# Optimization experiments

Hardware: AMD Instinct MI355X
Metric: run time of the kernel (lower is better)

Reference implementation:

```python
import jax, jax.numpy as jnp
import numpy as np


def setup_inputs() -> dict:
    key = jax.random.key(0)
    k1, k2, k3, k4, k5 = jax.random.split(key, 5)
    B, IN_N, POSE = 32, 8192, 64
    M = 8                     # matrix_pose_dim = sqrt(64)
    NH, S2, HID = 32, 256, 256  # in_n/(img^2), img^2, hidden_dim
    OUT_N = 64
    return {
        "current_pose": jax.random.normal(k1, (B, IN_N, POSE), jnp.float32),
        "w_current": 0.02 * jax.random.normal(k2, (1, 1, IN_N, M, M), jnp.float32),
        "w_next": 0.02 * jax.random.normal(k3, (OUT_N, M, M), jnp.float32),
        "E_proj": 0.02 * jax.random.normal(k4, (NH, S2, HID), jnp.float32),
        "rel_embedd": jax.random.normal(k5, (1, 1, POSE), jnp.float32),
    }


def reference(current_pose, w_current, w_next, E_proj, rel_embedd):
    B, IN_N, POSE = current_pose.shape
    M = w_current.shape[-1]           # matrix_pose_dim
    NH, S2, HID = E_proj.shape        # heads, img*img, hidden_dim
    OUT_N = w_next.shape[0]

    # w_current: (1,1,IN_N,M,M) -> (1,IN_N,M,M); per-capsule pose-matrix multiply
    wc = w_current.reshape(IN_N, M, M)[None]
    cp = current_pose.reshape(B, IN_N, M, M)
    cp = jnp.matmul(cp, wc)                      # (B, IN_N, M, M)

    # raw reshape (row-major, matches torch .reshape) then Linformer projection
    cp = cp.reshape(B, POSE, NH, 1, S2)
    cp = jnp.matmul(cp, E_proj)                  # (B, POSE, NH, 1, HID)
    cp = cp[:, :, :, 0, :]                       # squeeze(3) -> (B, POSE, NH, HID)
    cp = cp.reshape(B, NH * HID, POSE)           # raw reshape as in torch

    # dots = softmax over out_n axis of a constant tensor == uniform 1/OUT_N.
    # einsum('bij,bje->bie') with uniform dots == mean over j, broadcast over i.
    pooled = jnp.sum(cp, axis=1, keepdims=True) / OUT_N   # (B, 1, POSE)
    npc = jnp.broadcast_to(pooled, (B, OUT_N, POSE))

    # add relative embedding (h_out = w_out = output_img_size = 1)
    npc = npc.reshape(B, OUT_N, 1, 1, POSE) + rel_embedd  # (B,OUT_N,1,1,POSE)
    npc = jnp.transpose(npc, (0, 2, 3, 1, 4)).reshape(B, OUT_N, POSE)

    # next-layer pose-matrix multiply
    npc = npc.reshape(B, OUT_N, M, M)
    npc = jnp.matmul(npc, w_next[None])           # (B, OUT_N, M, M)
    npc = npc.reshape(B, 1, 1, OUT_N, POSE)
    return npc[:, 0]                              # squeeze(1) -> (B,1,OUT_N,POSE)
```

## Files before the change

kernel.cpp:

```cpp
#include <hip/hip_runtime.h>
#include <hip/hip_bf16.h>


typedef short short8_t __attribute__((ext_vector_type(8)));
typedef float f32x4_t __attribute__((ext_vector_type(4)));
typedef int   int4_t  __attribute__((ext_vector_type(4)));

__device__ __forceinline__ short f2bf(float f) {
    union { float f; unsigned u; } v; v.f = f;
    unsigned r = v.u + 0x7FFFu + ((v.u >> 16) & 1u);
    return (short)(r >> 16);
}

__device__ __forceinline__ int cvt_pk(float x, float y) {
    int r;
    asm("v_cvt_pk_bf16_f32 %0, %1, %2" : "=v"(r) : "v"(x), "v"(y));
    return r;
}

__global__ void k_prep(const float* __restrict__ WC, short* __restrict__ WCf,
                       const float* __restrict__ E, float* __restrict__ F) {
    if (blockIdx.x < 256) {
        int t   = blockIdx.x * 256 + threadIdx.x;
        int l   = t & 63;
        int pc  = (t >> 6) & 15;
        int rp  = t >> 10;
        int lhi = l >> 4;
        int j   = l & 15;
        int row = (pc * 4 + lhi) * 128 + rp * 2 + (j >> 3);
        const float* src = WC + ((size_t)row << 6) + (j & 7);
        short8_t o;
        #pragma unroll
        for (int k = 0; k < 8; ++k) o[k] = f2bf(src[k * 8]);
        ((short8_t*)WCf)[t] = o;
    } else {
        int idx = ((blockIdx.x - 256) * 256 + threadIdx.x) * 4;
        int q   = idx & 63;
        int row = idx >> 6;
        int r   = row >> 6;
        int e   = row & 63;
        int nh  = r >> 2;
        int s2  = ((r & 3) << 6) + e;
        const float* base = E + (((size_t)nh * 256 + s2) << 8) + q;
        float4 s0 = *(const float4*)(base);
        float4 s1 = *(const float4*)(base + 64);
        float4 s2v = *(const float4*)(base + 128);
        float4 s3 = *(const float4*)(base + 192);
        float4 o;
        o.x = s0.x + s1.x + s2v.x + s3.x;
        o.y = s0.y + s1.y + s2v.y + s3.y;
        o.z = s0.z + s1.z + s2v.z + s3.z;
        o.w = s0.w + s1.w + s2v.w + s3.w;
        *(float4*)(F + idx) = o;
    }
}

__global__ void __launch_bounds__(512, 4)
k_bc(const float* __restrict__ CP, const short* __restrict__ WCf,
     const float* __restrict__ F, float* __restrict__ P) {
    int gx   = blockIdx.x;
    int half = gx & 1;
    int rpg  = gx >> 1;
    int b0   = blockIdx.y * 2;
    int w = threadIdx.x >> 6;
    int l = threadIdx.x & 63;
    int b_loc  = w & 1;
    int rp_loc = w >> 1;
    int rp = rpg * 4 + rp_loc;
    int r0 = rp * 2;
    int b  = b0 + b_loc;

    int i16   = l & 15;
    int r_sel = i16 >> 3;
    int m1    = i16 & 7;
    int lhi   = l >> 4;

    __shared__ float Stile[2][512];
    __shared__ float redp[8][2][64];

    const float* cp_base = CP + ((size_t)b << 19) + ((size_t)(r0 + r_sel) << 6) + m1 * 8;
    const short8_t* wf   = (const short8_t*)WCf + (size_t)rp * 1024 + (half * 8) * 64 + l;

    short8_t wr0 = wf[0 * 64], wr1 = wf[1 * 64], wr2 = wf[2 * 64], wr3 = wf[3 * 64];
    short8_t wr4 = wf[4 * 64], wr5 = wf[5 * 64], wr6 = wf[6 * 64], wr7 = wf[7 * 64];

    const float* pbase = cp_base + (((size_t)(half * 8) * 4 + lhi) << 13);
    #define CPA(c) (pbase + ((size_t)((c) * 4) << 13))

    float4 a0A, a1A, b0A, b1A;
    float4 a0B, a1B, b0B, b1B;
    float4 a0C, a1C, b0C, b1C;
    float4 a0D, a1D, b0D, b1D;

    a0A = *(const float4*)(CPA(0));     a1A = *(const float4*)(CPA(0) + 4);
    b0A = *(const float4*)(CPA(1));     b1A = *(const float4*)(CPA(1) + 4);
    a0B = *(const float4*)(CPA(2));     a1B = *(const float4*)(CPA(2) + 4);
    b0B = *(const float4*)(CPA(3));     b1B = *(const float4*)(CPA(3) + 4);

    f32x4_t acc0 = {0.f, 0.f, 0.f, 0.f};
    f32x4_t acc1 = {0.f, 0.f, 0.f, 0.f};

    #define DO_PAIR(x0, x1, y0, y1, wlo, whi)                                  \
    {                                                                          \
        int4_t ai, bi;                                                         \
        ai[0] = cvt_pk(x0.x, x0.y); ai[1] = cvt_pk(x0.z, x0.w);                \
        ai[2] = cvt_pk(x1.x, x1.y); ai[3] = cvt_pk(x1.z, x1.w);                \
        bi[0] = cvt_pk(y0.x, y0.y); bi[1] = cvt_pk(y0.z, y0.w);                \
        bi[2] = cvt_pk(y1.x, y1.y); bi[3] = cvt_pk(y1.z, y1.w);                \
        acc0 = __builtin_amdgcn_mfma_f32_16x16x32_bf16(                        \
            __builtin_bit_cast(short8_t, ai), wlo, acc0, 0, 0, 0);             \
        acc1 = __builtin_amdgcn_mfma_f32_16x16x32_bf16(                        \
            __builtin_bit_cast(short8_t, bi), whi, acc1, 0, 0, 0);             \
    }

    a0C = *(const float4*)(CPA(4));     a1C = *(const float4*)(CPA(4) + 4);
    b0C = *(const float4*)(CPA(5));     b1C = *(const float4*)(CPA(5) + 4);
    DO_PAIR(a0A, a1A, b0A, b1A, wr0, wr1);
    a0D = *(const float4*)(CPA(6));     a1D = *(const float4*)(CPA(6) + 4);
    b0D = *(const float4*)(CPA(7));     b1D = *(const float4*)(CPA(7) + 4);
    DO_PAIR(a0B, a1B, b0B, b1B, wr2, wr3);
    DO_PAIR(a0C, a1C, b0C, b1C, wr4, wr5);
    DO_PAIR(a0D, a1D, b0D, b1D, wr6, wr7);
    #undef DO_PAIR
    #undef CPA

    f32x4_t acc;
    #pragma unroll
    for (int v = 0; v < 4; ++v) acc[v] = acc0[v] + acc1[v];

    int col = i16;
    #pragma unroll
    for (int v = 0; v < 4; ++v) {
        int row = lhi * 4 + v;
        if (row < 8 && col < 8)
            Stile[b_loc][rp_loc * 128 + row * 8 + col] = acc[v];
        else if (row >= 8 && col >= 8)
            Stile[b_loc][rp_loc * 128 + 64 + (row - 8) * 8 + (col - 8)] = acc[v];
    }
    __syncthreads();

    int g  = l >> 4;
    int ql = l & 15;
    const float* Fb = F + (((size_t)(rpg * 512 + w * 64 + g)) << 6) + ql * 4;
    f32x4_t p0 = {0.f, 0.f, 0.f, 0.f};
    f32x4_t p1 = {0.f, 0.f, 0.f, 0.f};
    #pragma unroll 4
    for (int s = 0; s < 16; ++s) {
        int jl = w * 64 + s * 4 + g;
        float4 fv = *(const float4*)(Fb + ((size_t)(s * 4) << 6));
        float s0 = Stile[0][jl];
        float s1 = Stile[1][jl];
        p0[0] += s0 * fv.x; p0[1] += s0 * fv.y; p0[2] += s0 * fv.z; p0[3] += s0 * fv.w;
        p1[0] += s1 * fv.x; p1[1] += s1 * fv.y; p1[2] += s1 * fv.z; p1[3] += s1 * fv.w;
    }
    #pragma unroll
    for (int c = 0; c < 4; ++c) {
        p0[c] += __shfl_xor(p0[c], 16, 64);
        p0[c] += __shfl_xor(p0[c], 32, 64);
        p1[c] += __shfl_xor(p1[c], 16, 64);
        p1[c] += __shfl_xor(p1[c], 32, 64);
    }
    if (l < 16) {
        *(f32x4_t*)(&redp[w][0][ql * 4]) = p0;
        *(f32x4_t*)(&redp[w][1][ql * 4]) = p1;
    }
    __syncthreads();

    if (threadIdx.x < 128) {
        int bb = threadIdx.x >> 6;
        int q  = threadIdx.x & 63;
        float s = 0.f;
        #pragma unroll
        for (int ww = 0; ww < 8; ++ww) s += redp[ww][bb][q];
        P[((size_t)((b0 + bb) * 32 + gx) << 6) + q] = s;
    }
}

__global__ void k_final(const float* __restrict__ P, const float* __restrict__ rel,
                        const float* __restrict__ WN, float* __restrict__ out) {
    int b  = blockIdx.x;
    int t  = threadIdx.x;
    int q    = t & 63;
    int sgrp = t >> 6;
    const float* Pb = P + ((size_t)(b * 32) << 6);
    float s = 0.f;
    #pragma unroll
    for (int c = sgrp * 8; c < sgrp * 8 + 8; ++c)
        s += Pb[((size_t)c << 6) + q];
    __shared__ float red[4][64];
    red[sgrp][q] = s;
    __syncthreads();
    __shared__ float pool_s[64];
    if (t < 64) {
        pool_s[t] = (red[0][t] + red[1][t] + red[2][t] + red[3][t]) * (1.0f / 64.0f)
                    + rel[t];
    }
    __syncthreads();
    #pragma unroll
    for (int idx = t; idx < 4096; idx += 256) {
        int o = idx >> 6;
        int e = idx & 63;
        int m1 = e >> 3, m2 = e & 7;
        float a = 0.f;
        #pragma unroll
        for (int k = 0; k < 8; ++k)
            a += pool_s[m1 * 8 + k] * WN[o * 64 + k * 8 + m2];
        out[((size_t)b << 12) + idx] = a;
    }
}

extern "C" void kernel_launch(void* const* d_in, const int* in_sizes, int n_in,
                              void* d_out, int out_size, void* d_ws, size_t ws_size,
                              hipStream_t stream) {
    const float* current_pose = (const float*)d_in[0];
    const float* w_current    = (const float*)d_in[1];
    const float* w_next       = (const float*)d_in[2];
    const float* E_proj       = (const float*)d_in[3];
    const float* rel_embedd   = (const float*)d_in[4];
    float* out = (float*)d_out;

    char* ws = (char*)d_ws;
    float* F   = (float*)(ws);
    short* WCf = (short*)(ws + (2u << 20));
    float* P   = (float*)(ws + (3u << 20));

    k_prep<<<dim3(768), dim3(256), 0, stream>>>(w_current, WCf, E_proj, F);
    k_bc<<<dim3(32, 16), dim3(512), 0, stream>>>(current_pose, WCf, F, P);
    k_final<<<dim3(32), dim3(256), 0, stream>>>(P, rel_embedd, w_next, out);
}
```

Before: 28.30 us.

## Fuse final reduction into main kernel via last-block atomic counter

Removes the separate k_final launch. Each k_bc block bumps a per-batch atomic counter after writing its partial sums, and the last block to arrive for a batch reduces the 32 partials, adds the embedding and applies the w_next matmul. This saves one kernel launch and its gap, at the cost of a threadfence, atomics and a serial tail inside a few blocks. The counters are never reset and rely on modulo-32 wraparound, so correctness depends on the workspace starting at a multiple of 32.

```diff
diff --git a/kernel.cpp b/kernel.cpp
--- a/kernel.cpp
+++ b/kernel.cpp
@@ -57,7 +57,9 @@
 
 __global__ void __launch_bounds__(512, 4)
 k_bc(const float* __restrict__ CP, const short* __restrict__ WCf,
-     const float* __restrict__ F, float* __restrict__ P) {
+     const float* __restrict__ F, const float* __restrict__ rel,
+     const float* __restrict__ WN, float* __restrict__ P,
+     unsigned* __restrict__ cnt, float* __restrict__ out) {
     int gx   = blockIdx.x;
     int half = gx & 1;
     int rpg  = gx >> 1;
@@ -77,6 +79,7 @@
 
     __shared__ float Stile[2][512];
     __shared__ float redp[8][2][64];
+    __shared__ int   winflag[2];
 
     const float* cp_base = CP + ((size_t)b << 19) + ((size_t)(r0 + r_sel) << 6) + m1 * 8;
     const short8_t* wf   = (const short8_t*)WCf + (size_t)rp * 1024 + (half * 8) * 64 + l;
@@ -174,38 +177,47 @@
         for (int ww = 0; ww < 8; ++ww) s += redp[ww][bb][q];
         P[((size_t)((b0 + bb) * 32 + gx) << 6) + q] = s;
     }
-}
-
-__global__ void k_final(const float* __restrict__ P, const float* __restrict__ rel,
-                        const float* __restrict__ WN, float* __restrict__ out) {
-    int b  = blockIdx.x;
-    int t  = threadIdx.x;
-    int q    = t & 63;
-    int sgrp = t >> 6;
-    const float* Pb = P + ((size_t)(b * 32) << 6);
-    float s = 0.f;
-    #pragma unroll
-    for (int c = sgrp * 8; c < sgrp * 8 + 8; ++c)
-        s += Pb[((size_t)c << 6) + q];
-    __shared__ float red[4][64];
-    red[sgrp][q] = s;
-    __syncthreads();
-    __shared__ float pool_s[64];
-    if (t < 64) {
-        pool_s[t] = (red[0][t] + red[1][t] + red[2][t] + red[3][t]) * (1.0f / 64.0f)
-                    + rel[t];
-    }
-    __syncthreads();
-    #pragma unroll
-    for (int idx = t; idx < 4096; idx += 256) {
-        int o = idx >> 6;
-        int e = idx & 63;
-        int m1 = e >> 3, m2 = e & 7;
-        float a = 0.f;
+
+    __threadfence();
+    __syncthreads();
+    if (threadIdx.x == 0) {
+        unsigned o0 = __hip_atomic_fetch_add(&cnt[(size_t)(b0 + 0) << 4], 1u,
+                                             __ATOMIC_ACQ_REL, __HIP_MEMORY_SCOPE_AGENT);
+        unsigned o1 = __hip_atomic_fetch_add(&cnt[(size_t)(b0 + 1) << 4], 1u,
+                                             __ATOMIC_ACQ_REL, __HIP_MEMORY_SCOPE_AGENT);
+        winflag[0] = ((o0 + 1u) & 31u) == 0u;
+        winflag[1] = ((o1 + 1u) & 31u) == 0u;
+    }
+    __syncthreads();
+
+    #pragma unroll
+    for (int bb = 0; bb < 2; ++bb) {
+        if (!winflag[bb]) continue;
+        int b_ = b0 + bb;
+        int q = threadIdx.x & 63, sg = threadIdx.x >> 6;
+        const float* Pb = P + ((size_t)(b_ * 32) << 6);
+        float s = 0.f;
         #pragma unroll
-        for (int k = 0; k < 8; ++k)
-            a += pool_s[m1 * 8 + k] * WN[o * 64 + k * 8 + m2];
-        out[((size_t)b << 12) + idx] = a;
+        for (int c = sg * 4; c < sg * 4 + 4; ++c)
+            s += Pb[((size_t)c << 6) + q];
+        redp[sg][0][q] = s;
+        __syncthreads();
+        if (threadIdx.x < 64) {
+            float ss = 0.f;
+            #pragma unroll
+            for (int gg = 0; gg < 8; ++gg) ss += redp[gg][0][threadIdx.x];
+            Stile[0][threadIdx.x] = ss * (1.0f / 64.0f) + rel[threadIdx.x];
+        }
+        __syncthreads();
+        for (int idx = threadIdx.x; idx < 4096; idx += 512) {
+            int o = idx >> 6, e = idx & 63, mm1 = e >> 3, mm2 = e & 7;
+            float a = 0.f;
+            #pragma unroll
+            for (int k = 0; k < 8; ++k)
+                a += Stile[0][mm1 * 8 + k] * WN[o * 64 + k * 8 + mm2];
+            out[((size_t)b_ << 12) + idx] = a;
+        }
+        __syncthreads();
     }
 }
 
@@ -220,11 +232,12 @@
     float* out = (float*)d_out;
 
     char* ws = (char*)d_ws;
-    float* F   = (float*)(ws);
-    short* WCf = (short*)(ws + (2u << 20));
-    float* P   = (float*)(ws + (3u << 20));
+    float*    F   = (float*)(ws);
+    short*    WCf = (short*)(ws + (2u << 20));
+    float*    P   = (float*)(ws + (3u << 20));
+    unsigned* cnt = (unsigned*)(ws + (3u << 20) + (1u << 19));
 
     k_prep<<<dim3(768), dim3(256), 0, stream>>>(w_current, WCf, E_proj, F);
-    k_bc<<<dim3(32, 16), dim3(512), 0, stream>>>(current_pose, WCf, F, P);
-    k_final<<<dim3(32), dim3(256), 0, stream>>>(P, rel_embedd, w_next, out);
-}
+    k_bc<<<dim3(32, 16), dim3(512), 0, stream>>>(current_pose, WCf, F, rel_embedd,
+                                                 w_next, P, cnt, out);
+}
```

Result: slower. 108.0 us (+281.7%).

## Move F-projection reduction into final kernel and store F and S in bf16

Applied to the files above, without the earlier changes.

The F-weighted projection, previously done per tile inside the main MFMA kernel with partial sums written to P, moves into a new per-batch final kernel. The main kernel now only writes the bf16 S matrix per half. The new final kernel sums the two halves, contracts against a bf16 copy of F over 8192 rows, then applies the w_next multiply. This cuts F traffic and shortens the main kernel. The cost is that the 8192-long reduction runs in only 32 blocks, which risks poor parallelism, and bf16 storage of S and F loses precision.

```diff
diff --git a/kernel.cpp b/kernel.cpp
--- a/kernel.cpp
+++ b/kernel.cpp
@@ -3,6 +3,7 @@
 
 
 typedef short short8_t __attribute__((ext_vector_type(8)));
+typedef short short4_t __attribute__((ext_vector_type(4)));
 typedef float f32x4_t __attribute__((ext_vector_type(4)));
 typedef int   int4_t  __attribute__((ext_vector_type(4)));
 
@@ -18,8 +19,12 @@
     return r;
 }
 
+__device__ __forceinline__ float bf2f(unsigned short u) {
+    union { float f; unsigned u; } v; v.u = ((unsigned)u) << 16; return v.f;
+}
+
 __global__ void k_prep(const float* __restrict__ WC, short* __restrict__ WCf,
-                       const float* __restrict__ E, float* __restrict__ F) {
+                       const float* __restrict__ E, short* __restrict__ F16) {
     if (blockIdx.x < 256) {
         int t   = blockIdx.x * 256 + threadIdx.x;
         int l   = t & 63;
@@ -46,18 +51,16 @@
         float4 s1 = *(const float4*)(base + 64);
         float4 s2v = *(const float4*)(base + 128);
         float4 s3 = *(const float4*)(base + 192);
-        float4 o;
-        o.x = s0.x + s1.x + s2v.x + s3.x;
-        o.y = s0.y + s1.y + s2v.y + s3.y;
-        o.z = s0.z + s1.z + s2v.z + s3.z;
-        o.w = s0.w + s1.w + s2v.w + s3.w;
-        *(float4*)(F + idx) = o;
+        int2 u;
+        u.x = cvt_pk(s0.x + s1.x + s2v.x + s3.x, s0.y + s1.y + s2v.y + s3.y);
+        u.y = cvt_pk(s0.z + s1.z + s2v.z + s3.z, s0.w + s1.w + s2v.w + s3.w);
+        *(int2*)(F16 + idx) = u;
     }
 }
 
 __global__ void __launch_bounds__(512, 4)
-k_bc(const float* __restrict__ CP, const short* __restrict__ WCf,
-     const float* __restrict__ F, float* __restrict__ P) {
+k_smat(const float* __restrict__ CP, const short* __restrict__ WCf,
+       short* __restrict__ Sh) {
     int gx   = blockIdx.x;
     int half = gx & 1;
     int rpg  = gx >> 1;
@@ -76,7 +79,6 @@
     int lhi   = l >> 4;
 
     __shared__ float Stile[2][512];
-    __shared__ float redp[8][2][64];
 
     const float* cp_base = CP + ((size_t)b << 19) + ((size_t)(r0 + r_sel) << 6) + m1 * 8;
     const short8_t* wf   = (const short8_t*)WCf + (size_t)rp * 1024 + (half * 8) * 64 + l;
@@ -139,68 +141,67 @@
     }
     __syncthreads();
 
-    int g  = l >> 4;
-    int ql = l & 15;
-    const float* Fb = F + (((size_t)(rpg * 512 + w * 64 + g)) << 6) + ql * 4;
-    f32x4_t p0 = {0.f, 0.f, 0.f, 0.f};
-    f32x4_t p1 = {0.f, 0.f, 0.f, 0.f};
-    #pragma unroll 4
-    for (int s = 0; s < 16; ++s) {
-        int jl = w * 64 + s * 4 + g;
-        float4 fv = *(const float4*)(Fb + ((size_t)(s * 4) << 6));
-        float s0 = Stile[0][jl];
-        float s1 = Stile[1][jl];
-        p0[0] += s0 * fv.x; p0[1] += s0 * fv.y; p0[2] += s0 * fv.z; p0[3] += s0 * fv.w;
-        p1[0] += s1 * fv.x; p1[1] += s1 * fv.y; p1[2] += s1 * fv.z; p1[3] += s1 * fv.w;
-    }
-    #pragma unroll
-    for (int c = 0; c < 4; ++c) {
-        p0[c] += __shfl_xor(p0[c], 16, 64);
-        p0[c] += __shfl_xor(p0[c], 32, 64);
-        p1[c] += __shfl_xor(p1[c], 16, 64);
-        p1[c] += __shfl_xor(p1[c], 32, 64);
-    }
-    if (l < 16) {
-        *(f32x4_t*)(&redp[w][0][ql * 4]) = p0;
-        *(f32x4_t*)(&redp[w][1][ql * 4]) = p1;
-    }
-    __syncthreads();
-
-    if (threadIdx.x < 128) {
-        int bb = threadIdx.x >> 6;
-        int q  = threadIdx.x & 63;
+    {
+        int tt  = threadIdx.x;
+        int bl  = tt >> 8;
+        int jl0 = (tt & 255) * 2;
+        int u = cvt_pk(Stile[bl][jl0], Stile[bl][jl0 + 1]);
+        *(int*)(Sh + (((size_t)(half * 32 + b0 + bl)) << 13) + rpg * 512 + jl0) = u;
+    }
+}
+
+__global__ void __launch_bounds__(512)
+k_pf(const short* __restrict__ Sh, const short* __restrict__ F16,
+     const float* __restrict__ rel, const float* __restrict__ WN,
+     float* __restrict__ out) {
+    int b = blockIdx.x;
+    int t = threadIdx.x;
+
+    __shared__ float Ssum[8192];
+    __shared__ float red2[32][64];
+    __shared__ float pool_s[64];
+
+    {
+        int j0 = t * 16;
+        #pragma unroll
+        for (int h = 0; h < 2; ++h) {
+            int j = j0 + h * 8;
+            short8_t v0 = *(const short8_t*)(Sh + ((size_t)(b) << 13) + j);
+            short8_t v1 = *(const short8_t*)(Sh + ((size_t)(32 + b) << 13) + j);
+            #pragma unroll
+            for (int k = 0; k < 8; ++k)
+                Ssum[j + k] = bf2f((unsigned short)v0[k]) + bf2f((unsigned short)v1[k]);
+        }
+    }
+    __syncthreads();
+
+    int ql = t & 15;
+    int jg = t >> 4;
+    f32x4_t acc = {0.f, 0.f, 0.f, 0.f};
+    const short* Fb = F16 + ql * 4;
+    #pragma unroll 8
+    for (int s = 0; s < 256; ++s) {
+        int j = s * 32 + jg;
+        float sv = Ssum[j];
+        short4_t fv = *(const short4_t*)(Fb + ((size_t)j << 6));
+        acc[0] += sv * bf2f((unsigned short)fv[0]);
+        acc[1] += sv * bf2f((unsigned short)fv[1]);
+        acc[2] += sv * bf2f((unsigned short)fv[2]);
+        acc[3] += sv * bf2f((unsigned short)fv[3]);
+    }
+    *(f32x4_t*)(&red2[jg][ql * 4]) = acc;
+    __syncthreads();
+
+    if (t < 64) {
         float s = 0.f;
         #pragma unroll
-        for (int ww = 0; ww < 8; ++ww) s += redp[ww][bb][q];
-        P[((size_t)((b0 + bb) * 32 + gx) << 6) + q] = s;
-    }
-}
-
-__global__ void k_final(const float* __restrict__ P, const float* __restrict__ rel,
-                        const float* __restrict__ WN, float* __restrict__ out) {
-    int b  = blockIdx.x;
-    int t  = threadIdx.x;
-    int q    = t & 63;
-    int sgrp = t >> 6;
-    const float* Pb = P + ((size_t)(b * 32) << 6);
-    float s = 0.f;
-    #pragma unroll
-    for (int c = sgrp * 8; c < sgrp * 8 + 8; ++c)
-        s += Pb[((size_t)c << 6) + q];
-    __shared__ float red[4][64];
-    red[sgrp][q] = s;
-    __syncthreads();
-    __shared__ float pool_s[64];
-    if (t < 64) {
-        pool_s[t] = (red[0][t] + red[1][t] + red[2][t] + red[3][t]) * (1.0f / 64.0f)
-                    + rel[t];
-    }
-    __syncthreads();
-    #pragma unroll
-    for (int idx = t; idx < 4096; idx += 256) {
-        int o = idx >> 6;
-        int e = idx & 63;
-        int m1 = e >> 3, m2 = e & 7;
+        for (int g = 0; g < 32; ++g) s += red2[g][t];
+        pool_s[t] = s * (1.0f / 64.0f) + rel[t];
+    }
+    __syncthreads();
+
+    for (int idx = t; idx < 4096; idx += 512) {
+        int o = idx >> 6, e = idx & 63, m1 = e >> 3, m2 = e & 7;
         float a = 0.f;
         #pragma unroll
         for (int k = 0; k < 8; ++k)
@@ -220,11 +221,11 @@
     float* out = (float*)d_out;
 
     char* ws = (char*)d_ws;
-    float* F   = (float*)(ws);
-    short* WCf = (short*)(ws + (2u << 20));
-    float* P   = (float*)(ws + (3u << 20));
-
-    k_prep<<<dim3(768), dim3(256), 0, stream>>>(w_current, WCf, E_proj, F);
-    k_bc<<<dim3(32, 16), dim3(512), 0, stream>>>(current_pose, WCf, F, P);
-    k_final<<<dim3(32), dim3(256), 0, stream>>>(P, rel_embedd, w_next, out);
-}
+    short* F16 = (short*)(ws);
+    short* WCf = (short*)(ws + (1u << 20));
+    short* Sh  = (short*)(ws + (2u << 20));
+
+    k_prep<<<dim3(768), dim3(256), 0, stream>>>(w_current, WCf, E_proj, F16);
+    k_smat<<<dim3(32, 16), dim3(512), 0, stream>>>(current_pose, WCf, Sh);
+    k_pf<<<dim3(32), dim3(512), 0, stream>>>(Sh, F16, rel_embedd, w_next, out);
+}
```

New measurement: 48.55 us. +71.6%, slower.

## Stream pose tiles via direct global-to-LDS loads with double buffering

Applied to the files above, without the earlier changes.

Replaces the register float4 loads of current_pose in k_bc with direct global_load_lds transfers into a per-wave LDS staging buffer. Explicit vmcnt waits and scheduling barriers pipeline the issue of later chunks with the bf16 conversion and MFMA on earlier ones. The aim is to cut VGPR pressure and keep more loads in flight. In exchange it adds 64KB of LDS per block, which may limit blocks per CU. It also adds an extra LDS read pass and a full vmcnt wait on the weight loads before streaming starts.

```diff
diff --git a/kernel.cpp b/kernel.cpp
--- a/kernel.cpp
+++ b/kernel.cpp
@@ -75,6 +75,7 @@
     int m1    = i16 & 7;
     int lhi   = l >> 4;
 
+    __shared__ float gbuf[8][2048];
     __shared__ float Stile[2][512];
     __shared__ float redp[8][2][64];
 
@@ -83,45 +84,60 @@
 
     short8_t wr0 = wf[0 * 64], wr1 = wf[1 * 64], wr2 = wf[2 * 64], wr3 = wf[3 * 64];
     short8_t wr4 = wf[4 * 64], wr5 = wf[5 * 64], wr6 = wf[6 * 64], wr7 = wf[7 * 64];
+    asm volatile("" :: "v"(wr0), "v"(wr1), "v"(wr2), "v"(wr3),
+                       "v"(wr4), "v"(wr5), "v"(wr6), "v"(wr7));
+    asm volatile("s_waitcnt vmcnt(0)" ::: "memory");
+    __builtin_amdgcn_sched_barrier(0);
+
+    int wu = __builtin_amdgcn_readfirstlane(w);
+    float* gb = &gbuf[wu][0];
 
     const float* pbase = cp_base + (((size_t)(half * 8) * 4 + lhi) << 13);
     #define CPA(c) (pbase + ((size_t)((c) * 4) << 13))
 
-    float4 a0A, a1A, b0A, b1A;
-    float4 a0B, a1B, b0B, b1B;
-    float4 a0C, a1C, b0C, b1C;
-    float4 a0D, a1D, b0D, b1D;
-
-    a0A = *(const float4*)(CPA(0));     a1A = *(const float4*)(CPA(0) + 4);
-    b0A = *(const float4*)(CPA(1));     b1A = *(const float4*)(CPA(1) + 4);
-    a0B = *(const float4*)(CPA(2));     a1B = *(const float4*)(CPA(2) + 4);
-    b0B = *(const float4*)(CPA(3));     b1B = *(const float4*)(CPA(3) + 4);
+    #define ISSUE(c, off) do {                                                        \
+        __builtin_amdgcn_global_load_lds((const void*)(CPA(c)),                       \
+                                         (void*)(gb + (off)), 16, 0, 0);              \
+        __builtin_amdgcn_global_load_lds((const void*)(CPA(c) + 4),                   \
+                                         (void*)(gb + (off) + 256), 16, 0, 0);        \
+    } while (0)
+
+    #define WAITVM(N) do {                                                            \
+        asm volatile("s_waitcnt vmcnt(" #N ")" ::: "memory");                         \
+        __builtin_amdgcn_sched_barrier(0);                                            \
+    } while (0)
 
     f32x4_t acc0 = {0.f, 0.f, 0.f, 0.f};
     f32x4_t acc1 = {0.f, 0.f, 0.f, 0.f};
 
-    #define DO_PAIR(x0, x1, y0, y1, wlo, whi)                                  \
-    {                                                                          \
-        int4_t ai, bi;                                                         \
-        ai[0] = cvt_pk(x0.x, x0.y); ai[1] = cvt_pk(x0.z, x0.w);                \
-        ai[2] = cvt_pk(x1.x, x1.y); ai[3] = cvt_pk(x1.z, x1.w);                \
-        bi[0] = cvt_pk(y0.x, y0.y); bi[1] = cvt_pk(y0.z, y0.w);                \
-        bi[2] = cvt_pk(y1.x, y1.y); bi[3] = cvt_pk(y1.z, y1.w);                \
-        acc0 = __builtin_amdgcn_mfma_f32_16x16x32_bf16(                        \
-            __builtin_bit_cast(short8_t, ai), wlo, acc0, 0, 0, 0);             \
-        acc1 = __builtin_amdgcn_mfma_f32_16x16x32_bf16(                        \
-            __builtin_bit_cast(short8_t, bi), whi, acc1, 0, 0, 0);             \
-    }
-
-    a0C = *(const float4*)(CPA(4));     a1C = *(const float4*)(CPA(4) + 4);
-    b0C = *(const float4*)(CPA(5));     b1C = *(const float4*)(CPA(5) + 4);
-    DO_PAIR(a0A, a1A, b0A, b1A, wr0, wr1);
-    a0D = *(const float4*)(CPA(6));     a1D = *(const float4*)(CPA(6) + 4);
-    b0D = *(const float4*)(CPA(7));     b1D = *(const float4*)(CPA(7) + 4);
-    DO_PAIR(a0B, a1B, b0B, b1B, wr2, wr3);
-    DO_PAIR(a0C, a1C, b0C, b1C, wr4, wr5);
-    DO_PAIR(a0D, a1D, b0D, b1D, wr6, wr7);
-    #undef DO_PAIR
+    #define COMPUTE(off, wfr, accX) do {                                              \
+        float4 x0 = *(const float4*)(gb + (off) + (size_t)l * 4);                     \
+        float4 x1 = *(const float4*)(gb + (off) + 256 + (size_t)l * 4);               \
+        int4_t ai;                                                                    \
+        ai[0] = cvt_pk(x0.x, x0.y); ai[1] = cvt_pk(x0.z, x0.w);                       \
+        ai[2] = cvt_pk(x1.x, x1.y); ai[3] = cvt_pk(x1.z, x1.w);                       \
+        accX = __builtin_amdgcn_mfma_f32_16x16x32_bf16(                               \
+            __builtin_bit_cast(short8_t, ai), wfr, accX, 0, 0, 0);                    \
+    } while (0)
+
+    ISSUE(0, 0);    ISSUE(1, 512);
+    ISSUE(2, 1024); ISSUE(3, 1536);
+    WAITVM(4);
+    COMPUTE(0, wr0, acc0); COMPUTE(512, wr1, acc1);
+    __builtin_amdgcn_sched_barrier(0);
+    ISSUE(4, 0);    ISSUE(5, 512);
+    WAITVM(4);
+    COMPUTE(1024, wr2, acc0); COMPUTE(1536, wr3, acc1);
+    __builtin_amdgcn_sched_barrier(0);
+    ISSUE(6, 1024); ISSUE(7, 1536);
+    WAITVM(4);
+    COMPUTE(0, wr4, acc0); COMPUTE(512, wr5, acc1);
+    WAITVM(0);
+    COMPUTE(1024, wr6, acc0); COMPUTE(1536, wr7, acc1);
+
+    #undef COMPUTE
+    #undef WAITVM
+    #undef ISSUE
     #undef CPA
 
     f32x4_t acc;
```

New measurement: 27.79 us. No clear change (-1.8%).
